# Kernel tuning notes

Measured on AMD Instinct MI355X. Metric: run time of the kernel, lower is better.

## Reference

```python
import jax, jax.numpy as jnp
import numpy as np

D_MODEL, D_INNER, D_STATE, D_CONV, DT_RANK = 1024, 2048, 16, 4, 64
BATCH, SEQLEN = 4, 2048


def setup_inputs() -> dict:
    key = jax.random.key(0)
    ks = jax.random.split(key, 10)
    def n(k, shape, scale=1.0):
        return (jax.random.normal(k, shape, dtype=jnp.float32) * scale)
    # A_log = log of positive values in (0, d_state] like the torch init
    A_log = jnp.log(jax.random.uniform(ks[7], (D_INNER, D_STATE), dtype=jnp.float32, minval=0.5, maxval=float(D_STATE)))
    return {
        "hidden_states": n(ks[0], (BATCH, SEQLEN, D_MODEL)),
        "in_proj_w": n(ks[1], (2 * D_INNER, D_MODEL), D_MODEL ** -0.5),
        "conv_w": n(ks[2], (D_INNER, D_CONV), D_CONV ** -0.5),
        "conv_b": n(ks[3], (D_INNER,), 0.1),
        "x_proj_w": n(ks[4], (DT_RANK + 2 * D_STATE, D_INNER), D_INNER ** -0.5),
        "dt_proj_w": n(ks[5], (D_INNER, DT_RANK), DT_RANK ** -0.5),
        "dt_proj_b": n(ks[6], (D_INNER,), 0.5),
        "A_log": A_log,
        "D": jnp.ones((D_INNER,), dtype=jnp.float32),
        "out_proj_w": n(ks[8], (D_MODEL, D_INNER), D_INNER ** -0.5),
    }


def _silu(x):
    return x * jax.nn.sigmoid(x)


def _mamba_forward(hidden_states, in_proj_w, conv_w, conv_b, x_proj_w,
                   dt_proj_w, dt_proj_b, A_log, D, out_proj_w):
    B, L, _ = hidden_states.shape
    d_inner, d_conv = conv_w.shape
    d_state = A_log.shape[1]
    dt_rank = dt_proj_w.shape[1]

    # in_proj (no bias): (b, l, 2*d_inner)
    xz = jnp.einsum('bld,ed->ble', hidden_states, in_proj_w)
    x, z = xz[..., :d_inner], xz[..., d_inner:]

    # causal depthwise conv1d (padding = d_conv-1, truncated to L) + SiLU
    x_pad = jnp.pad(x, ((0, 0), (d_conv - 1, 0), (0, 0)))  # (b, L+d_conv-1, d)
    x_conv = sum(x_pad[:, w:w + L, :] * conv_w[:, w] for w in range(d_conv)) + conv_b
    x_conv = _silu(x_conv)  # (b, l, d_inner)

    # x_proj -> dt, B, C
    x_dbl = jnp.einsum('bld,ed->ble', x_conv, x_proj_w)  # (b, l, dt_rank+2*d_state)
    dt_in = x_dbl[..., :dt_rank]
    Bv = x_dbl[..., dt_rank:dt_rank + d_state]  # (b, l, n)
    Cv = x_dbl[..., dt_rank + d_state:]         # (b, l, n)

    delta = jax.nn.softplus(jnp.einsum('blr,dr->bld', dt_in, dt_proj_w) + dt_proj_b)
    A = -jnp.exp(A_log)  # (d, n), entries negative

    # selective scan over time: state h is (b, d, n)
    def step(h, inp):
        d_t, B_t, C_t, u_t = inp  # (b,d), (b,n), (b,n), (b,d)
        dA = jnp.exp(d_t[:, :, None] * A)                          # (b, d, n)
        h = h * dA + (d_t * u_t)[:, :, None] * B_t[:, None, :]     # (b, d, n)
        y = jnp.einsum('bdn,bn->bd', h, C_t)                       # (b, d)
        return h, y

    h0 = jnp.zeros((B, d_inner, d_state), dtype=hidden_states.dtype)
    xs = (jnp.swapaxes(delta, 0, 1), jnp.swapaxes(Bv, 0, 1),
          jnp.swapaxes(Cv, 0, 1), jnp.swapaxes(x_conv, 0, 1))
    _, ys = jax.lax.scan(step, h0, xs)  # (l, b, d)
    y = jnp.swapaxes(ys, 0, 1) + x_conv * D  # skip term D * u
    y = y * _silu(z)                           # gating

    # out_proj (no bias)
    return jnp.einsum('bld,md->blm', y, out_proj_w)


def reference(hidden_states, in_proj_w, conv_w, conv_b, x_proj_w,
              dt_proj_w, dt_proj_b, A_log, D, out_proj_w):
    return _mamba_forward(hidden_states, in_proj_w, conv_w, conv_b, x_proj_w,
                          dt_proj_w, dt_proj_b, A_log, D, out_proj_w)
```

## Files before the change

### kernel.cpp

```cpp
#include <hip/hip_runtime.h>
#include <hip/hip_bf16.h>

constexpr int BATCH = 4, SEQLEN = 2048, DM = 1024, DI = 2048, DS = 16, DC = 4, DTR = 64;
constexpr int M = BATCH * SEQLEN;
constexpr int NXZ = 2 * DI;
constexpr int NXDBL = DTR + 2 * DS;
constexpr int CL = 64;
constexpr int NCH = SEQLEN / CL;
constexpr size_t CS = (size_t)BATCH * DI * DS;
constexpr float L2E = 1.44269504088896f;

typedef __attribute__((ext_vector_type(8))) short short8;
typedef __attribute__((ext_vector_type(4))) float f32x4;

__device__ __forceinline__ float fexp2(float x) { return __builtin_amdgcn_exp2f(x); }
__device__ __forceinline__ float frcp(float x) { return __builtin_amdgcn_rcpf(x); }
__device__ __forceinline__ float fsig(float z) {
  return frcp(1.f + fexp2(-L2E * z));
}
__device__ __forceinline__ float softplus_fast(float x) {
  return (x > 20.f) ? x
                    : 0.693147180559945f * __builtin_amdgcn_logf(1.f + fexp2(x * L2E));
}

__device__ __forceinline__ void load_lds16(const void* g, void* l) {
  __builtin_amdgcn_global_load_lds(
      (const __attribute__((address_space(1))) unsigned int*)g,
      (__attribute__((address_space(3))) unsigned int*)l, 16, 0, 0);
}

__global__ __launch_bounds__(256) void k_cvt(const float* __restrict__ s,
                                             __hip_bfloat16* __restrict__ d, int n) {
  int i = (blockIdx.x * 256 + threadIdx.x) * 4;
  if (i + 3 < n) {
    float4 v = *reinterpret_cast<const float4*>(s + i);
    d[i + 0] = __float2bfloat16(v.x);
    d[i + 1] = __float2bfloat16(v.y);
    d[i + 2] = __float2bfloat16(v.z);
    d[i + 3] = __float2bfloat16(v.w);
  }
}

__global__ __launch_bounds__(256) void k_cvt4(const float* __restrict__ p0, int n0, __hip_bfloat16* __restrict__ q0,
                                              const float* __restrict__ p1, int n1, __hip_bfloat16* __restrict__ q1,
                                              const float* __restrict__ p2, int n2, __hip_bfloat16* __restrict__ q2,
                                              const float* __restrict__ p3, int n3, __hip_bfloat16* __restrict__ q3) {
  int i = (blockIdx.x * 256 + threadIdx.x) * 4;
  const float* s;
  __hip_bfloat16* d;
  if (i < n0) { s = p0; d = q0; }
  else if ((i -= n0) < n1) { s = p1; d = q1; }
  else if ((i -= n1) < n2) { s = p2; d = q2; }
  else if ((i -= n2) < n3) { s = p3; d = q3; }
  else return;
  float4 v = *reinterpret_cast<const float4*>(s + i);
  d[i + 0] = __float2bfloat16(v.x);
  d[i + 1] = __float2bfloat16(v.y);
  d[i + 2] = __float2bfloat16(v.z);
  d[i + 3] = __float2bfloat16(v.w);
}

__global__ __launch_bounds__(256) void k_prepA(const float* __restrict__ alog,
                                               float* __restrict__ an, int n) {
  int i = blockIdx.x * 256 + threadIdx.x;
  if (i < n) an[i] = -__expf(alog[i]) * L2E;
}

__global__ __launch_bounds__(256) void k_prepCW(const float* __restrict__ cw,
                                                float* __restrict__ cwt) {
  int i = blockIdx.x * 256 + threadIdx.x;
  if (i < DI * DC) {
    int d = i >> 2, w = i & 3;
    cwt[w * DI + d] = cw[i];
  }
}

template <int BN, int OUTMODE, bool SWZ>
__global__ __launch_bounds__(512, 2) void k_gemmp(const __hip_bfloat16* __restrict__ A, int lda,
                                                  const __hip_bfloat16* __restrict__ Bm, int ldb,
                                                  void* __restrict__ Cp, int ldc, int K) {
  constexpr int BK = 64;
  constexpr int ASLOT = 16384;
  constexpr int BSLOT = BN * BK;
  constexpr int FN = (BN / 4) / 16;
  constexpr int BBASE = 2 * ASLOT;

  const int tid = threadIdx.x;
  const int wid = tid >> 6, l = tid & 63;
  const int wr = wid >> 2, wc = wid & 3;

  int bx = blockIdx.x, by = blockIdx.y;
  if constexpr (SWZ) {
    const int gx = gridDim.x;
    int nlin = by * gx + bx;
    const int nwg = gx * gridDim.y;
    nlin = (nlin & 7) * (nwg >> 3) + (nlin >> 3);
    by = nlin / gx; bx = nlin % gx;
  }
  const int bm0 = by * 256, bn0 = bx * BN;
  const int NT = K / BK;

  __shared__ short LDS[2 * (ASLOT + BSLOT)];

  const int gc8 = (l & 7) ^ ((l >> 3) & 7);
  const __hip_bfloat16* Abase = A + (size_t)(bm0 + wid * 8 + (l >> 3)) * lda + gc8 * 8;
  const __hip_bfloat16* Bbase = Bm + (size_t)(bn0 + wid * 8 + (l >> 3)) * ldb + gc8 * 8;
  const int wslot = wid * 512;

  const int c8k0 = ((l >> 4) ^ (l & 7)) * 8;
  const int c8k1 = ((4 + (l >> 4)) ^ (l & 7)) * 8;
  const int aoff0 = wr * 8192 + (l & 15) * 64;
  const int boff0 = BBASE + wc * (BN / 4) * 64 + (l & 15) * 64;

  f32x4 acc[8][FN] = {};

  auto stageA = [&](int s, int kt) {
#pragma unroll
    for (int g = 0; g < 4; g++)
      load_lds16(Abase + (size_t)(g * 64) * lda + kt * BK,
                 &LDS[s * ASLOT + g * 4096 + wslot]);
  };
  auto stageB = [&](int s, int kt) {
#pragma unroll
    for (int g = 0; g < BN / 64; g++)
      load_lds16(Bbase + (size_t)(g * 64) * ldb + kt * BK,
                 &LDS[BBASE + s * BSLOT + g * 4096 + wslot]);
  };

  stageA(0, 0); stageB(0, 0);

  for (int t = 0; t < NT; t++) {
    const int d = t & 1;
    asm volatile("s_waitcnt vmcnt(0)" ::: "memory");
    __builtin_amdgcn_s_barrier();
    if (t + 1 < NT) { stageA(d ^ 1, t + 1); stageB(d ^ 1, t + 1); }

    const int adb = d * ASLOT + aoff0;
    const int bdb = d * BSLOT + boff0;
    short8 a0[4][2], a1[4][2], b[FN][2];
#pragma unroll
    for (int i = 0; i < 4; i++) {
      a0[i][0] = *reinterpret_cast<const short8*>(&LDS[adb + i * 1024 + c8k0]);
      a0[i][1] = *reinterpret_cast<const short8*>(&LDS[adb + i * 1024 + c8k1]);
    }
#pragma unroll
    for (int j = 0; j < FN; j++) {
      b[j][0] = *reinterpret_cast<const short8*>(&LDS[bdb + j * 1024 + c8k0]);
      b[j][1] = *reinterpret_cast<const short8*>(&LDS[bdb + j * 1024 + c8k1]);
    }
#pragma unroll
    for (int i = 0; i < 4; i++) {
      a1[i][0] = *reinterpret_cast<const short8*>(&LDS[adb + (4 + i) * 1024 + c8k0]);
      a1[i][1] = *reinterpret_cast<const short8*>(&LDS[adb + (4 + i) * 1024 + c8k1]);
    }
#pragma unroll
    for (int i = 0; i < 4; i++)
#pragma unroll
      for (int j = 0; j < FN; j++)
#pragma unroll
        for (int ks = 0; ks < 2; ks++) {
          acc[i][j] = __builtin_amdgcn_mfma_f32_16x16x32_bf16(a0[i][ks], b[j][ks], acc[i][j], 0, 0, 0);
          acc[4 + i][j] = __builtin_amdgcn_mfma_f32_16x16x32_bf16(a1[i][ks], b[j][ks], acc[4 + i][j], 0, 0, 0);
        }
  }

  const int crow0 = bm0 + wr * 128 + (l >> 4) * 4;
  const int ccol0 = bn0 + wc * (BN / 4) + (l & 15);
#pragma unroll
  for (int im = 0; im < 8; im++)
#pragma unroll
    for (int jn = 0; jn < FN; jn++) {
      const int col = ccol0 + jn * 16;
#pragma unroll
      for (int r = 0; r < 4; r++) {
        const int row = crow0 + im * 16 + r;
        float v = acc[im][jn][r];
        if constexpr (OUTMODE == 0)
          reinterpret_cast<float*>(Cp)[(size_t)row * ldc + col] = v;
        else
          reinterpret_cast<__hip_bfloat16*>(Cp)[(size_t)row * ldc + col] = __float2bfloat16(v);
      }
    }
}

template <int BM, int BN, int OUTMODE>
__global__ __launch_bounds__(256) void k_gemm_dl(const __hip_bfloat16* __restrict__ A, int lda,
                                                 const __hip_bfloat16* __restrict__ Bm, int ldb,
                                                 void* __restrict__ Cp, int ldc, int K,
                                                 const float* __restrict__ bias) {
  constexpr int BK = 32;
  constexpr int WM = BM / 2, WN = BN / 2;
  constexpr int FM = WM / 16, FN = WN / 16;

  const int tid = threadIdx.x;
  const int wid = tid >> 6, lane = tid & 63;
  const int wm = wid >> 1, wn = wid & 1;
  const int bm0 = blockIdx.y * BM, bn0 = blockIdx.x * BN;
  int kz = 0;
  if constexpr (OUTMODE == 4) kz = blockIdx.z;

  __shared__ short As[BM * BK];
  __shared__ short Bs[BN * BK];

  f32x4 acc[FM][FN] = {};

  const int lrow = lane & 15;
  const int lk = (lane >> 4) * 8;
  const int srow = wid * 16 + (lane >> 2);
  const int scol = (lane & 3) * 8;

  const __hip_bfloat16* Ag = &A[(size_t)(bm0 + srow) * lda + scol + (size_t)kz * K];
  const __hip_bfloat16* Bg = &Bm[(size_t)(bn0 + srow) * ldb + scol + (size_t)kz * K];

  for (int k0 = 0; k0 < K; k0 += BK) {
    __syncthreads();
#pragma unroll
    for (int i = 0; i < (BM + 63) / 64; i++)
      load_lds16(Ag + (size_t)i * 64 * lda + k0, &As[(i * 64 + wid * 16) * BK]);
#pragma unroll
    for (int i = 0; i < (BN + 63) / 64; i++)
      if ((BN % 64 == 0) || (i * 64 + wid * 16 < BN))
        load_lds16(Bg + (size_t)i * 64 * ldb + k0, &Bs[(i * 64 + wid * 16) * BK]);
    __syncthreads();

    short8 af[FM], bf[FN];
#pragma unroll
    for (int i = 0; i < FM; i++)
      af[i] = *reinterpret_cast<const short8*>(&As[(wm * WM + i * 16 + lrow) * BK + lk]);
#pragma unroll
    for (int j = 0; j < FN; j++)
      bf[j] = *reinterpret_cast<const short8*>(&Bs[(wn * WN + j * 16 + lrow) * BK + lk]);
#pragma unroll
    for (int i = 0; i < FM; i++)
#pragma unroll
      for (int j = 0; j < FN; j++)
        acc[i][j] = __builtin_amdgcn_mfma_f32_16x16x32_bf16(af[i], bf[j], acc[i][j], 0, 0, 0);
  }

  const int crow0 = bm0 + wm * WM + (lane >> 4) * 4;
  const int ccol0 = bn0 + wn * WN + lrow;
#pragma unroll
  for (int i = 0; i < FM; i++)
#pragma unroll
    for (int j = 0; j < FN; j++) {
      const int col = ccol0 + j * 16;
      float bv = 0.f;
      if constexpr (OUTMODE == 2) bv = bias[col];
#pragma unroll
      for (int r = 0; r < 4; r++) {
        const int row = crow0 + i * 16 + r;
        float v = acc[i][j][r];
        if constexpr (OUTMODE == 0) {
          reinterpret_cast<float*>(Cp)[(size_t)row * ldc + col] = v;
        } else if constexpr (OUTMODE == 2) {
          reinterpret_cast<__hip_bfloat16*>(Cp)[(size_t)row * ldc + col] =
              __float2bfloat16(softplus_fast(v + bv));
        } else {
          reinterpret_cast<float*>(Cp)[(size_t)kz * M * NXDBL + (size_t)row * ldc + col] = v;
        }
      }
    }
}

__global__ __launch_bounds__(256) void k_xred(const float* __restrict__ part,
                                              float* __restrict__ xdbl,
                                              __hip_bfloat16* __restrict__ dtin) {
  int i = (blockIdx.x * 256 + threadIdx.x) * 4;
  float4 s = *reinterpret_cast<const float4*>(part + i);
#pragma unroll
  for (int p = 1; p < 8; p++) {
    const float4 v = *reinterpret_cast<const float4*>(part + (size_t)p * M * NXDBL + i);
    s.x += v.x; s.y += v.y; s.z += v.z; s.w += v.w;
  }
  *reinterpret_cast<float4*>(xdbl + i) = s;
  int c = i % NXDBL;
  if (c < DTR) {
    int m = i / NXDBL;
    __hip_bfloat16* dp = dtin + (size_t)m * DTR + c;
    dp[0] = __float2bfloat16(s.x);
    dp[1] = __float2bfloat16(s.y);
    dp[2] = __float2bfloat16(s.z);
    dp[3] = __float2bfloat16(s.w);
  }
}

__global__ __launch_bounds__(256) void k_conv8(const __hip_bfloat16* __restrict__ xz,
                                               const float* __restrict__ cwt,
                                               const float* __restrict__ cb,
                                               __hip_bfloat16* __restrict__ xc) {
  const int ml = blockIdx.x;
  const int d0 = threadIdx.x * 8;
  const int l = ml & (SEQLEN - 1);
  float acc[8];
  {
    float4 b0 = *reinterpret_cast<const float4*>(cb + d0);
    float4 b1 = *reinterpret_cast<const float4*>(cb + d0 + 4);
    acc[0] = b0.x; acc[1] = b0.y; acc[2] = b0.z; acc[3] = b0.w;
    acc[4] = b1.x; acc[5] = b1.y; acc[6] = b1.z; acc[7] = b1.w;
  }
#pragma unroll
  for (int w = 0; w < DC; w++) {
    int li = l - 3 + w;
    if (li >= 0) {
      short8 xv = *reinterpret_cast<const short8*>(&xz[(size_t)(ml - 3 + w) * NXZ + d0]);
      float4 w0 = *reinterpret_cast<const float4*>(cwt + w * DI + d0);
      float4 w1 = *reinterpret_cast<const float4*>(cwt + w * DI + d0 + 4);
      float wf[8] = {w0.x, w0.y, w0.z, w0.w, w1.x, w1.y, w1.z, w1.w};
#pragma unroll
      for (int j = 0; j < 8; j++) {
        float x = __bfloat162float(__ushort_as_bfloat16((unsigned short)xv[j]));
        acc[j] = fmaf(x, wf[j], acc[j]);
      }
    }
  }
  unsigned short o[8];
#pragma unroll
  for (int j = 0; j < 8; j++)
    o[j] = __bfloat16_as_ushort(__float2bfloat16(acc[j] * fsig(acc[j])));
  *reinterpret_cast<short8*>(&xc[(size_t)ml * DI + d0]) = *reinterpret_cast<short8*>(o);
}

__global__ __launch_bounds__(256) void k_scan1(const __hip_bfloat16* __restrict__ delta_b,
                                               const float* __restrict__ xdbl,
                                               const __hip_bfloat16* __restrict__ xc,
                                               const float* __restrict__ Aneg2,
                                               __hip_bfloat16* __restrict__ Pb,
                                               __hip_bfloat16* __restrict__ Sb) {
  const int tid = threadIdx.x;
  const int d = blockIdx.x * 256 + tid;
  const int c = blockIdx.y, b = blockIdx.z;
  const size_t row0 = (size_t)b * SEQLEN + (size_t)c * CL;

  __shared__ float Bs[CL][16];
  {
    int i = tid * 4;
    int li = i >> 4, n0 = i & 15;
    const float* src = &xdbl[(row0 + li) * NXDBL + DTR + n0];
    *reinterpret_cast<float4*>(&Bs[li][n0]) = *reinterpret_cast<const float4*>(src);
  }

  float Ar[DS];
#pragma unroll
  for (int n = 0; n < DS; n++) Ar[n] = Aneg2[d * DS + n];
  __syncthreads();

  float h[DS] = {};
  float sdelta = 0.f;
  size_t idx = row0 * DI + d;
  float nx_dt = __bfloat162float(delta_b[idx]);
  float nx_u = __bfloat162float(xc[idx]);
  for (int ls = 0; ls < CL; ls++) {
    float delta = nx_dt;
    float u = nx_u;
    if (ls + 1 < CL) {
      size_t idx2 = idx + DI;
      nx_dt = __bfloat162float(delta_b[idx2]);
      nx_u = __bfloat162float(xc[idx2]);
    }
    idx += DI;
    sdelta += delta;
    float du = delta * u;
#pragma unroll
    for (int n = 0; n < DS; n++) {
      float dA = fexp2(delta * Ar[n]);
      h[n] = fmaf(h[n], dA, du * Bs[ls][n]);
    }
  }

  size_t base = (size_t)c * CS + ((size_t)b * DI + d) * DS;
  unsigned short sp[DS], ss[DS];
#pragma unroll
  for (int n = 0; n < DS; n++) {
    ss[n] = __bfloat16_as_ushort(__float2bfloat16(h[n]));
    sp[n] = __bfloat16_as_ushort(__float2bfloat16(fexp2(Ar[n] * sdelta)));
  }
#pragma unroll
  for (int q = 0; q < 2; q++) {
    *reinterpret_cast<short8*>(&Sb[base + q * 8]) = *reinterpret_cast<short8*>(&ss[q * 8]);
    *reinterpret_cast<short8*>(&Pb[base + q * 8]) = *reinterpret_cast<short8*>(&sp[q * 8]);
  }
}

__global__ __launch_bounds__(256) void k_scan2(const __hip_bfloat16* __restrict__ Pb,
                                               const __hip_bfloat16* __restrict__ Sb,
                                               __hip_bfloat16* __restrict__ Hin) {
  size_t t = (size_t)blockIdx.x * 256 + threadIdx.x;
  float h = 0.f;
  for (int c = 0; c < NCH; c++) {
    size_t o = (size_t)c * CS + t;
    Hin[o] = __float2bfloat16(h);
    h = fmaf(__bfloat162float(Pb[o]), h, __bfloat162float(Sb[o]));
  }
}

__global__ __launch_bounds__(256) void k_scan3(const __hip_bfloat16* __restrict__ delta_b,
                                               const float* __restrict__ xdbl,
                                               const __hip_bfloat16* __restrict__ xc,
                                               const __hip_bfloat16* __restrict__ xz,
                                               const float* __restrict__ Aneg2,
                                               const float* __restrict__ Dw,
                                               const __hip_bfloat16* __restrict__ Hin,
                                               __hip_bfloat16* __restrict__ yg) {
  const int tid = threadIdx.x;
  const int d = blockIdx.x * 256 + tid;
  const int c = blockIdx.y, b = blockIdx.z;
  const size_t row0 = (size_t)b * SEQLEN + (size_t)c * CL;

  __shared__ float BCs[CL][32];
  {
    int i = tid * 8;
    int li = i >> 5, n0 = i & 31;
    const float* src = &xdbl[(row0 + li) * NXDBL + DTR + n0];
    *reinterpret_cast<float4*>(&BCs[li][n0]) = *reinterpret_cast<const float4*>(src);
    *reinterpret_cast<float4*>(&BCs[li][n0 + 4]) = *reinterpret_cast<const float4*>(src + 4);
  }

  float Ar[DS];
#pragma unroll
  for (int n = 0; n < DS; n++) Ar[n] = Aneg2[d * DS + n];
  const float Dv = Dw[d];

  float h[DS];
  {
    size_t hbase = (size_t)c * CS + ((size_t)b * DI + d) * DS;
#pragma unroll
    for (int q = 0; q < 2; q++) {
      short8 hv = *reinterpret_cast<const short8*>(&Hin[hbase + q * 8]);
#pragma unroll
      for (int n = 0; n < 8; n++)
        h[q * 8 + n] = __bfloat162float(__ushort_as_bfloat16((unsigned short)hv[n]));
    }
  }
  __syncthreads();

  size_t idx = row0 * DI + d;
  float nx_dt = __bfloat162float(delta_b[idx]);
  float nx_u = __bfloat162float(xc[idx]);
  float nx_z = __bfloat162float(xz[row0 * NXZ + DI + d]);
  for (int ls = 0; ls < CL; ls++) {
    const size_t cur = idx;
    float delta = nx_dt;
    float u = nx_u;
    float zv = nx_z;
    if (ls + 1 < CL) {
      size_t idx2 = idx + DI;
      nx_dt = __bfloat162float(delta_b[idx2]);
      nx_u = __bfloat162float(xc[idx2]);
      nx_z = __bfloat162float(xz[(row0 + ls + 1) * NXZ + DI + d]);
    }
    idx += DI;
    float du = delta * u;
    float y0 = 0.f, y1 = 0.f, y2 = 0.f, y3 = 0.f;
#pragma unroll
    for (int q = 0; q < 4; q++) {
#pragma unroll
      for (int n4 = 0; n4 < 4; n4++) {
        const int n = q * 4 + n4;
        float dA = fexp2(delta * Ar[n]);
        h[n] = fmaf(h[n], dA, du * BCs[ls][n]);
        if (q == 0) y0 = fmaf(h[n], BCs[ls][16 + n], y0);
        else if (q == 1) y1 = fmaf(h[n], BCs[ls][16 + n], y1);
        else if (q == 2) y2 = fmaf(h[n], BCs[ls][16 + n], y2);
        else y3 = fmaf(h[n], BCs[ls][16 + n], y3);
      }
    }
    float y = (y0 + y1) + (y2 + y3);
    float out = (y + u * Dv) * (zv * fsig(zv));
    yg[cur] = __float2bfloat16(out);
  }
}

extern "C" void kernel_launch(void* const* d_in, const int* in_sizes, int n_in,
                              void* d_out, int out_size, void* d_ws, size_t ws_size,
                              hipStream_t stream) {
  const float* hs = (const float*)d_in[0];
  const float* w_in = (const float*)d_in[1];
  const float* conv_w = (const float*)d_in[2];
  const float* conv_b = (const float*)d_in[3];
  const float* w_xp = (const float*)d_in[4];
  const float* w_dt = (const float*)d_in[5];
  const float* dt_b = (const float*)d_in[6];
  const float* A_log = (const float*)d_in[7];
  const float* Dw = (const float*)d_in[8];
  const float* w_out = (const float*)d_in[9];
  float* out = (float*)d_out;

  char* ws = (char*)d_ws;
  size_t off = 0;
  auto alloc = [&](size_t bytes) {
    void* p = ws + off;
    off += (bytes + 255) & ~(size_t)255;
    return p;
  };

  __hip_bfloat16* hs_b   = (__hip_bfloat16*)alloc((size_t)M * DM * 2);
  __hip_bfloat16* win_b  = (__hip_bfloat16*)alloc((size_t)NXZ * DM * 2);
  __hip_bfloat16* wxp_b  = (__hip_bfloat16*)alloc((size_t)NXDBL * DI * 2);
  __hip_bfloat16* wdt_b  = (__hip_bfloat16*)alloc((size_t)DI * DTR * 2);
  __hip_bfloat16* wout_b = (__hip_bfloat16*)alloc((size_t)DM * DI * 2);
  float*          Aneg2  = (float*)alloc((size_t)DI * DS * 4);
  float*          cwt    = (float*)alloc((size_t)DC * DI * 4);
  __hip_bfloat16* xz_b   = (__hip_bfloat16*)alloc((size_t)M * NXZ * 2);
  __hip_bfloat16* xc_b   = (__hip_bfloat16*)alloc((size_t)M * DI * 2);
  float*          xdbl   = (float*)alloc((size_t)M * NXDBL * 4);
  __hip_bfloat16* dtin_b = (__hip_bfloat16*)alloc((size_t)M * DTR * 2);
  __hip_bfloat16* delta_b= (__hip_bfloat16*)alloc((size_t)M * DI * 2);
  __hip_bfloat16* yg_b   = (__hip_bfloat16*)alloc((size_t)M * DI * 2);

  float* xpart = (float*)(ws + 0);
  __hip_bfloat16* Pb  = (__hip_bfloat16*)(ws + 0);
  __hip_bfloat16* Sb  = (__hip_bfloat16*)(ws + ((size_t)8 << 20));
  __hip_bfloat16* Hin = (__hip_bfloat16*)(ws + ((size_t)16 << 20));

  k_cvt<<<(M * DM) / 1024, 256, 0, stream>>>(hs, hs_b, M * DM);
  k_cvt4<<<(NXZ * DM + NXDBL * DI + DI * DTR + DM * DI) / 1024, 256, 0, stream>>>(
      w_in, NXZ * DM, win_b, w_xp, NXDBL * DI, wxp_b, w_dt, DI * DTR, wdt_b,
      w_out, DM * DI, wout_b);
  k_prepA<<<(DI * DS) / 256, 256, 0, stream>>>(A_log, Aneg2, DI * DS);
  k_prepCW<<<(DI * DC + 255) / 256, 256, 0, stream>>>(conv_w, cwt);

  k_gemmp<256, 1, false><<<dim3(NXZ / 256, M / 256), 512, 0, stream>>>(
      hs_b, DM, win_b, DM, xz_b, NXZ, DM);

  k_conv8<<<M, 256, 0, stream>>>(xz_b, cwt, conv_b, xc_b);

  k_gemm_dl<64, 96, 4><<<dim3(1, M / 64, 8), 256, 0, stream>>>(
      xc_b, DI, wxp_b, DI, xpart, NXDBL, DI / 8, nullptr);
  k_xred<<<(M * NXDBL) / 1024, 256, 0, stream>>>(xpart, xdbl, dtin_b);

  k_gemm_dl<128, 128, 2><<<dim3(DI / 128, M / 128), 256, 0, stream>>>(
      dtin_b, DTR, wdt_b, DTR, delta_b, DI, DTR, dt_b);

  k_scan1<<<dim3(DI / 256, NCH, BATCH), 256, 0, stream>>>(delta_b, xdbl, xc_b,
                                                          Aneg2, Pb, Sb);
  k_scan2<<<(int)(CS / 256), 256, 0, stream>>>(Pb, Sb, Hin);
  k_scan3<<<dim3(DI / 256, NCH, BATCH), 256, 0, stream>>>(delta_b, xdbl, xc_b,
                                                          xz_b, Aneg2, Dw, Hin, yg_b);

  k_gemmp<128, 0, true><<<dim3(DM / 128, M / 256), 512, 0, stream>>>(
      yg_b, DI, wout_b, DI, out, DM, DI);
}
```

Measured before the change: 300.0 us.

## Triple-buffer GEMM pipeline with BK=32 and widen bf16 conversion stores

Reworks the main bf16 MFMA GEMM from a double-buffered BK=64 loop to a three-stage LDS ring with BK=32, issuing loads two tiles ahead and waiting with partial vmcnt so global-to-LDS copies overlap compute. It adds a new swizzle for the narrower tile, raises wave priority around the MFMA block and uses sched_barrier. The fp32-to-bf16 conversion kernels now handle 8 elements per thread with a single 16-byte store. The cost is more barriers per K step and hand-tuned vmcnt counts that must match the number of issued loads.

```diff
diff --git a/kernel.cpp b/kernel.cpp
--- a/kernel.cpp
+++ b/kernel.cpp
@@ -31,13 +31,20 @@
 
 __global__ __launch_bounds__(256) void k_cvt(const float* __restrict__ s,
                                              __hip_bfloat16* __restrict__ d, int n) {
-  int i = (blockIdx.x * 256 + threadIdx.x) * 4;
-  if (i + 3 < n) {
-    float4 v = *reinterpret_cast<const float4*>(s + i);
-    d[i + 0] = __float2bfloat16(v.x);
-    d[i + 1] = __float2bfloat16(v.y);
-    d[i + 2] = __float2bfloat16(v.z);
-    d[i + 3] = __float2bfloat16(v.w);
+  int i = (blockIdx.x * 256 + threadIdx.x) * 8;
+  if (i + 7 < n) {
+    float4 v0 = *reinterpret_cast<const float4*>(s + i);
+    float4 v1 = *reinterpret_cast<const float4*>(s + i + 4);
+    unsigned short o[8];
+    o[0] = __bfloat16_as_ushort(__float2bfloat16(v0.x));
+    o[1] = __bfloat16_as_ushort(__float2bfloat16(v0.y));
+    o[2] = __bfloat16_as_ushort(__float2bfloat16(v0.z));
+    o[3] = __bfloat16_as_ushort(__float2bfloat16(v0.w));
+    o[4] = __bfloat16_as_ushort(__float2bfloat16(v1.x));
+    o[5] = __bfloat16_as_ushort(__float2bfloat16(v1.y));
+    o[6] = __bfloat16_as_ushort(__float2bfloat16(v1.z));
+    o[7] = __bfloat16_as_ushort(__float2bfloat16(v1.w));
+    *reinterpret_cast<short8*>(d + i) = *reinterpret_cast<short8*>(o);
   }
 }
 
@@ -45,7 +52,7 @@
                                               const float* __restrict__ p1, int n1, __hip_bfloat16* __restrict__ q1,
                                               const float* __restrict__ p2, int n2, __hip_bfloat16* __restrict__ q2,
                                               const float* __restrict__ p3, int n3, __hip_bfloat16* __restrict__ q3) {
-  int i = (blockIdx.x * 256 + threadIdx.x) * 4;
+  int i = (blockIdx.x * 256 + threadIdx.x) * 8;
   const float* s;
   __hip_bfloat16* d;
   if (i < n0) { s = p0; d = q0; }
@@ -53,11 +60,18 @@
   else if ((i -= n1) < n2) { s = p2; d = q2; }
   else if ((i -= n2) < n3) { s = p3; d = q3; }
   else return;
-  float4 v = *reinterpret_cast<const float4*>(s + i);
-  d[i + 0] = __float2bfloat16(v.x);
-  d[i + 1] = __float2bfloat16(v.y);
-  d[i + 2] = __float2bfloat16(v.z);
-  d[i + 3] = __float2bfloat16(v.w);
+  float4 v0 = *reinterpret_cast<const float4*>(s + i);
+  float4 v1 = *reinterpret_cast<const float4*>(s + i + 4);
+  unsigned short o[8];
+  o[0] = __bfloat16_as_ushort(__float2bfloat16(v0.x));
+  o[1] = __bfloat16_as_ushort(__float2bfloat16(v0.y));
+  o[2] = __bfloat16_as_ushort(__float2bfloat16(v0.z));
+  o[3] = __bfloat16_as_ushort(__float2bfloat16(v0.w));
+  o[4] = __bfloat16_as_ushort(__float2bfloat16(v1.x));
+  o[5] = __bfloat16_as_ushort(__float2bfloat16(v1.y));
+  o[6] = __bfloat16_as_ushort(__float2bfloat16(v1.z));
+  o[7] = __bfloat16_as_ushort(__float2bfloat16(v1.w));
+  *reinterpret_cast<short8*>(d + i) = *reinterpret_cast<short8*>(o);
 }
 
 __global__ __launch_bounds__(256) void k_prepA(const float* __restrict__ alog,
@@ -76,14 +90,14 @@
 }
 
 template <int BN, int OUTMODE, bool SWZ>
-__global__ __launch_bounds__(512, 2) void k_gemmp(const __hip_bfloat16* __restrict__ A, int lda,
+__global__ __launch_bounds__(512, 2) void k_gemm3(const __hip_bfloat16* __restrict__ A, int lda,
                                                   const __hip_bfloat16* __restrict__ Bm, int ldb,
                                                   void* __restrict__ Cp, int ldc, int K) {
-  constexpr int BK = 64;
-  constexpr int ASLOT = 16384;
-  constexpr int BSLOT = BN * BK;
-  constexpr int FN = (BN / 4) / 16;
-  constexpr int BBASE = 2 * ASLOT;
+  constexpr int BK = 32;
+  constexpr int ASL = 256 * BK;
+  constexpr int BSL = BN * BK;
+  constexpr int SLOT = ASL + BSL;
+  constexpr int FN = BN / 64;
 
   const int tid = threadIdx.x;
   const int wid = tid >> 6, l = tid & 63;
@@ -100,68 +114,67 @@
   const int bm0 = by * 256, bn0 = bx * BN;
   const int NT = K / BK;
 
-  __shared__ short LDS[2 * (ASLOT + BSLOT)];
-
-  const int gc8 = (l & 7) ^ ((l >> 3) & 7);
-  const __hip_bfloat16* Abase = A + (size_t)(bm0 + wid * 8 + (l >> 3)) * lda + gc8 * 8;
-  const __hip_bfloat16* Bbase = Bm + (size_t)(bn0 + wid * 8 + (l >> 3)) * ldb + gc8 * 8;
-  const int wslot = wid * 512;
-
-  const int c8k0 = ((l >> 4) ^ (l & 7)) * 8;
-  const int c8k1 = ((4 + (l >> 4)) ^ (l & 7)) * 8;
-  const int aoff0 = wr * 8192 + (l & 15) * 64;
-  const int boff0 = BBASE + wc * (BN / 4) * 64 + (l & 15) * 64;
+  __shared__ short LDS[3 * SLOT];
+
+  const int srow = tid >> 2;
+  const int sc8 = ((tid & 3) ^ ((srow >> 1) & 3)) * 8;
+  const __hip_bfloat16* Abase = A + (size_t)(bm0 + srow) * lda + sc8;
+  const __hip_bfloat16* Bbase = Bm + (size_t)(bn0 + srow) * ldb + sc8;
+  const int wdst = wid * 512;
+
+  const int cp8 = ((l >> 4) ^ (((l & 15) >> 1) & 3)) * 8;
+  const int abase_l = (wr * 128 + (l & 15)) * BK + cp8;
+  const int bbase_l = ASL + (wc * (BN / 4) + (l & 15)) * BK + cp8;
 
   f32x4 acc[8][FN] = {};
 
   auto stageA = [&](int s, int kt) {
 #pragma unroll
-    for (int g = 0; g < 4; g++)
-      load_lds16(Abase + (size_t)(g * 64) * lda + kt * BK,
-                 &LDS[s * ASLOT + g * 4096 + wslot]);
+    for (int g = 0; g < 2; g++)
+      load_lds16(Abase + (size_t)(g * 128) * lda + kt * BK,
+                 &LDS[s * SLOT + g * 4096 + wdst]);
   };
   auto stageB = [&](int s, int kt) {
 #pragma unroll
-    for (int g = 0; g < BN / 64; g++)
-      load_lds16(Bbase + (size_t)(g * 64) * ldb + kt * BK,
-                 &LDS[BBASE + s * BSLOT + g * 4096 + wslot]);
+    for (int g = 0; g < BN / 128; g++)
+      load_lds16(Bbase + (size_t)(g * 128) * ldb + kt * BK,
+                 &LDS[s * SLOT + ASL + g * 4096 + wdst]);
   };
 
   stageA(0, 0); stageB(0, 0);
+  if (NT > 1) { stageA(1, 1); stageB(1, 1); }
 
   for (int t = 0; t < NT; t++) {
-    const int d = t & 1;
-    asm volatile("s_waitcnt vmcnt(0)" ::: "memory");
+    const int s = t % 3;
+    if (t + 1 < NT) {
+      if constexpr (BN == 256) asm volatile("s_waitcnt vmcnt(4)" ::: "memory");
+      else                     asm volatile("s_waitcnt vmcnt(3)" ::: "memory");
+    } else {
+      asm volatile("s_waitcnt vmcnt(0)" ::: "memory");
+    }
     __builtin_amdgcn_s_barrier();
-    if (t + 1 < NT) { stageA(d ^ 1, t + 1); stageB(d ^ 1, t + 1); }
-
-    const int adb = d * ASLOT + aoff0;
-    const int bdb = d * BSLOT + boff0;
-    short8 a0[4][2], a1[4][2], b[FN][2];
-#pragma unroll
-    for (int i = 0; i < 4; i++) {
-      a0[i][0] = *reinterpret_cast<const short8*>(&LDS[adb + i * 1024 + c8k0]);
-      a0[i][1] = *reinterpret_cast<const short8*>(&LDS[adb + i * 1024 + c8k1]);
-    }
-#pragma unroll
-    for (int j = 0; j < FN; j++) {
-      b[j][0] = *reinterpret_cast<const short8*>(&LDS[bdb + j * 1024 + c8k0]);
-      b[j][1] = *reinterpret_cast<const short8*>(&LDS[bdb + j * 1024 + c8k1]);
-    }
-#pragma unroll
-    for (int i = 0; i < 4; i++) {
-      a1[i][0] = *reinterpret_cast<const short8*>(&LDS[adb + (4 + i) * 1024 + c8k0]);
-      a1[i][1] = *reinterpret_cast<const short8*>(&LDS[adb + (4 + i) * 1024 + c8k1]);
-    }
-#pragma unroll
-    for (int i = 0; i < 4; i++)
+    __builtin_amdgcn_sched_barrier(0);
+    if (t + 2 < NT) {
+      const int s2 = (t + 2) % 3;
+      stageA(s2, t + 2);
+      stageB(s2, t + 2);
+    }
+    const int ab = s * SLOT + abase_l;
+    const int bb = s * SLOT + bbase_l;
+    short8 a[8], b[FN];
+#pragma unroll
+    for (int i = 0; i < 8; i++)
+      a[i] = *reinterpret_cast<const short8*>(&LDS[ab + i * 512]);
+#pragma unroll
+    for (int j = 0; j < FN; j++)
+      b[j] = *reinterpret_cast<const short8*>(&LDS[bb + j * 512]);
+    __builtin_amdgcn_s_setprio(1);
+#pragma unroll
+    for (int i = 0; i < 8; i++)
 #pragma unroll
       for (int j = 0; j < FN; j++)
-#pragma unroll
-        for (int ks = 0; ks < 2; ks++) {
-          acc[i][j] = __builtin_amdgcn_mfma_f32_16x16x32_bf16(a0[i][ks], b[j][ks], acc[i][j], 0, 0, 0);
-          acc[4 + i][j] = __builtin_amdgcn_mfma_f32_16x16x32_bf16(a1[i][ks], b[j][ks], acc[4 + i][j], 0, 0, 0);
-        }
+        acc[i][j] = __builtin_amdgcn_mfma_f32_16x16x32_bf16(a[i], b[j], acc[i][j], 0, 0, 0);
+    __builtin_amdgcn_s_setprio(0);
   }
 
   const int crow0 = bm0 + wr * 128 + (l >> 4) * 4;
@@ -512,14 +525,14 @@
   __hip_bfloat16* Sb  = (__hip_bfloat16*)(ws + ((size_t)8 << 20));
   __hip_bfloat16* Hin = (__hip_bfloat16*)(ws + ((size_t)16 << 20));
 
-  k_cvt<<<(M * DM) / 1024, 256, 0, stream>>>(hs, hs_b, M * DM);
-  k_cvt4<<<(NXZ * DM + NXDBL * DI + DI * DTR + DM * DI) / 1024, 256, 0, stream>>>(
+  k_cvt<<<(M * DM) / 2048, 256, 0, stream>>>(hs, hs_b, M * DM);
+  k_cvt4<<<(NXZ * DM + NXDBL * DI + DI * DTR + DM * DI) / 2048, 256, 0, stream>>>(
       w_in, NXZ * DM, win_b, w_xp, NXDBL * DI, wxp_b, w_dt, DI * DTR, wdt_b,
       w_out, DM * DI, wout_b);
   k_prepA<<<(DI * DS) / 256, 256, 0, stream>>>(A_log, Aneg2, DI * DS);
   k_prepCW<<<(DI * DC + 255) / 256, 256, 0, stream>>>(conv_w, cwt);
 
-  k_gemmp<256, 1, false><<<dim3(NXZ / 256, M / 256), 512, 0, stream>>>(
+  k_gemm3<256, 1, false><<<dim3(NXZ / 256, M / 256), 512, 0, stream>>>(
       hs_b, DM, win_b, DM, xz_b, NXZ, DM);
 
   k_conv8<<<M, 256, 0, stream>>>(xz_b, cwt, conv_b, xc_b);
@@ -537,6 +550,6 @@
   k_scan3<<<dim3(DI / 256, NCH, BATCH), 256, 0, stream>>>(delta_b, xdbl, xc_b,
                                                           xz_b, Aneg2, Dw, Hin, yg_b);
 
-  k_gemmp<128, 0, true><<<dim3(DM / 128, M / 256), 512, 0, stream>>>(
+  k_gemm3<128, 0, true><<<dim3(DM / 128, M / 256), 512, 0, stream>>>(
       yg_b, DI, wout_b, DI, out, DM, DI);
 }
```

Result: slower. 310.1 us (+3.4%).
